# Performance work log

Hardware: AMD Instinct MI355X
Metric: run time of the kernel (lower is better)

## Reference

```python
import jax, jax.numpy as jnp
import numpy as np

EPS = 1e-12  # torch F.normalize eps

def _normalize(x):
    # L2-normalize along last dim, matching F.normalize(dim=-1)
    n = jnp.linalg.norm(x, axis=-1, keepdims=True)
    return x / jnp.maximum(n, EPS)

def setup_inputs() -> dict:
    key = jax.random.key(0)
    k1, k2, k3 = jax.random.split(key, 3)
    B, K, D = 32768, 8, 256
    return {
        "drone_slots": jax.random.normal(k1, (B, K, D), dtype=jnp.float32),
        "sat_slots": jax.random.normal(k2, (B, K, D), dtype=jnp.float32),
        "labels": jax.random.randint(k3, (B,), 0, 1000, dtype=jnp.int64),
        "temperature": 0.1,
    }

def reference(drone_slots, sat_slots, labels, temperature):
    # labels are unused by the original math (targets are arange(K))
    ds = _normalize(drone_slots)  # [B,K,D]
    ss = _normalize(sat_slots)    # [B,K,D]
    logits = jnp.einsum("bkd,bjd->bkj", ds, ss) / temperature  # [B,K,K]
    # cross_entropy with targets = arange(K): positive is the diagonal
    lse = jax.nn.logsumexp(logits, axis=-1)                      # [B,K]
    pos = jnp.diagonal(logits, axis1=-2, axis2=-1)               # [B,K]
    ce_per_sample = jnp.mean(lse - pos, axis=-1)                 # [B], per-sample mean-reduced CE
    return jnp.mean(ce_per_sample)                               # average over batch
```

## Files before the change

kernel.cpp:

```cpp
#include <hip/hip_runtime.h>
#include <hip/hip_bf16.h>


typedef __attribute__((ext_vector_type(8))) short bf16x8;
typedef __attribute__((ext_vector_type(4))) float f32x4;

union BFPack { bf16x8 v; __hip_bfloat162 h[4]; };

__device__ inline bf16x8 pack8(const float4& lo, const float4& hi) {
  BFPack u;
  u.h[0] = __float22bfloat162_rn(make_float2(lo.x, lo.y));
  u.h[1] = __float22bfloat162_rn(make_float2(lo.z, lo.w));
  u.h[2] = __float22bfloat162_rn(make_float2(hi.x, hi.y));
  u.h[3] = __float22bfloat162_rn(make_float2(hi.z, hi.w));
  return u.v;
}

extern "C" __global__ __launch_bounds__(256, 2)
void slot_ce_mfma(const float* __restrict__ ds, const float* __restrict__ ss,
                  const float* __restrict__ tptr, float* __restrict__ ws,
                  int ntiles) {
  const int lane = threadIdx.x & 63;
  const int wid  = blockIdx.x * 4 + (threadIdx.x >> 6);
  const int m = lane & 15;
  const int h = lane >> 4;
  const float inv_t = 1.0f / tptr[0];

  float loss = 0.0f;

  if (wid < ntiles) {
    const float4* pa = (const float4*)(ds + (size_t)wid * 4096);
    const float4* pb = (const float4*)(ss + (size_t)wid * 4096);
    const int base = m * 64 + h * 2;

    float4 A[16], S[16];
#pragma unroll
    for (int kb = 0; kb < 8; ++kb) {
      A[2 * kb]     = pa[base + kb * 8];
      A[2 * kb + 1] = pa[base + kb * 8 + 1];
      S[2 * kb]     = pb[base + kb * 8];
      S[2 * kb + 1] = pb[base + kb * 8 + 1];
    }

    f32x4 acc = {0.f, 0.f, 0.f, 0.f};
    float ssqA = 0.f, ssqS = 0.f;
#pragma unroll
    for (int kb = 0; kb < 8; ++kb) {
      float4 a0 = A[2 * kb], a1 = A[2 * kb + 1];
      float4 s0 = S[2 * kb], s1 = S[2 * kb + 1];

      ssqA += a0.x*a0.x + a0.y*a0.y + a0.z*a0.z + a0.w*a0.w
            + a1.x*a1.x + a1.y*a1.y + a1.z*a1.z + a1.w*a1.w;
      ssqS += s0.x*s0.x + s0.y*s0.y + s0.z*s0.z + s0.w*s0.w
            + s1.x*s1.x + s1.y*s1.y + s1.z*s1.z + s1.w*s1.w;

      acc = __builtin_amdgcn_mfma_f32_16x16x32_bf16(
          pack8(a0, a1), pack8(s0, s1), acc, 0, 0, 0);
    }

    ssqA += __shfl_xor(ssqA, 16, 64);
    ssqA += __shfl_xor(ssqA, 32, 64);
    ssqS += __shfl_xor(ssqS, 16, 64);
    ssqS += __shfl_xor(ssqS, 32, 64);
    float na0 = __shfl(ssqA, h * 4 + 0, 64);
    float na1 = __shfl(ssqA, h * 4 + 1, 64);
    float na2 = __shfl(ssqA, h * 4 + 2, 64);
    float na3 = __shfl(ssqA, h * 4 + 3, 64);

    float lg0 = acc[0] * rsqrtf(na0 * ssqS) * inv_t;
    float lg1 = acc[1] * rsqrtf(na1 * ssqS) * inv_t;
    float lg2 = acc[2] * rsqrtf(na2 * ssqS) * inv_t;
    float lg3 = acc[3] * rsqrtf(na3 * ssqS) * inv_t;

    float c = 0.0f;
#pragma unroll
    for (int r = 0; r < 4; ++r) {
      float lg = r == 0 ? lg0 : r == 1 ? lg1 : r == 2 ? lg2 : lg3;
      float mx = lg;
      mx = fmaxf(mx, __shfl_xor(mx, 1, 64));
      mx = fmaxf(mx, __shfl_xor(mx, 2, 64));
      mx = fmaxf(mx, __shfl_xor(mx, 4, 64));
      float e = __expf(lg - mx);
      e += __shfl_xor(e, 1, 64);
      e += __shfl_xor(e, 2, 64);
      e += __shfl_xor(e, 4, 64);
      float lse = mx + __logf(e);
      c += lse * 0.125f;
      if (4 * h + r == m) c -= lg;
    }
    if ((m >= 8) == (h >= 2)) loss = c;
  }

#pragma unroll
  for (int o = 32; o >= 1; o >>= 1) loss += __shfl_xor(loss, o, 64);
  __shared__ float red[4];
  if (lane == 0) red[threadIdx.x >> 6] = loss;
  __syncthreads();
  if (threadIdx.x == 0)
    ws[blockIdx.x] = (red[0] + red[1]) + (red[2] + red[3]);
}

extern "C" __global__ __launch_bounds__(256)
void slot_ce_finish(const float* __restrict__ ws, float* __restrict__ out,
                    int nparts, float scale) {
  __shared__ float red[256];
  float s = 0.0f;
  for (int i = threadIdx.x; i < nparts; i += 256) s += ws[i];
  red[threadIdx.x] = s;
  __syncthreads();
  for (int o = 128; o >= 1; o >>= 1) {
    if ((int)threadIdx.x < o) red[threadIdx.x] += red[threadIdx.x + o];
    __syncthreads();
  }
  if (threadIdx.x == 0) out[0] = red[0] * scale;
}

extern "C" void kernel_launch(void* const* d_in, const int* in_sizes, int n_in,
                              void* d_out, int out_size, void* d_ws, size_t ws_size,
                              hipStream_t stream) {
  const float* ds   = (const float*)d_in[0];
  const float* ss   = (const float*)d_in[1];
  const float* tptr = (const float*)d_in[3];
  float* out = (float*)d_out;
  float* ws  = (float*)d_ws;

  const int B      = in_sizes[0] / (8 * 256);
  const int ntiles = B / 2;
  const int blocks = (ntiles + 3) / 4;

  slot_ce_mfma<<<blocks, 256, 0, stream>>>(ds, ss, tptr, ws, ntiles);
  const float scale = 1.0f / (8.0f * (float)B);
  slot_ce_finish<<<1, 256, 0, stream>>>(ws, out, blocks, scale);
}
```

Baseline: 106.5 us.

## Stage slot tiles through LDS via direct global-to-LDS loads and fuse final reduction

Replaces the register-held 32 float4 loads per lane with global_load_lds transfers into a swizzled per-wave LDS region, processing the 256-wide dimension in four chunks and raising launch bounds to 5 blocks per CU. The final cross-block reduction is folded into the main kernel with an atomic ticket counter so the last block sums the partials, which drops the second launch but adds a memset. The per-chunk load then wait-for-all-loads pattern serializes memory and compute within a wave and relies on occupancy to hide latency. The LDS reads are missing a wait before the final chunk is consumed, and reuse of the buffer between chunks depends on manual waitcnt placement.

```diff
diff --git a/kernel.cpp b/kernel.cpp
--- a/kernel.cpp
+++ b/kernel.cpp
@@ -16,46 +16,69 @@
   return u.v;
 }
 
-extern "C" __global__ __launch_bounds__(256, 2)
-void slot_ce_mfma(const float* __restrict__ ds, const float* __restrict__ ss,
-                  const float* __restrict__ tptr, float* __restrict__ ws,
-                  int ntiles) {
-  const int lane = threadIdx.x & 63;
-  const int wid  = blockIdx.x * 4 + (threadIdx.x >> 6);
-  const int m = lane & 15;
-  const int h = lane >> 4;
+#define GLL16(gaddr, laddr)                                                    \
+  __builtin_amdgcn_global_load_lds(                                            \
+      (const __attribute__((address_space(1))) void*)(gaddr),                  \
+      (__attribute__((address_space(3))) void*)(laddr), 16, 0, 0)
+
+extern "C" __global__ __launch_bounds__(256, 5)
+void slot_ce_fused(const float* __restrict__ ds, const float* __restrict__ ss,
+                   const float* __restrict__ tptr, float* __restrict__ ws,
+                   unsigned* __restrict__ counter, float* __restrict__ out,
+                   int ntiles, int nblocks, float scale) {
+  __shared__ char lds[32768];
+  const int tid  = threadIdx.x;
+  const int lane = tid & 63;
+  const int wv   = tid >> 6;
+  const int wid  = blockIdx.x * 4 + wv;
+  const int m  = lane & 15;
+  const int h  = lane >> 4;
   const float inv_t = 1.0f / tptr[0];
 
+  char* wreg = &lds[wv * 8192];
   float loss = 0.0f;
 
   if (wid < ntiles) {
-    const float4* pa = (const float4*)(ds + (size_t)wid * 4096);
-    const float4* pb = (const float4*)(ss + (size_t)wid * 4096);
-    const int base = m * 64 + h * 2;
+    const char* gA = (const char*)ds + (size_t)wid * 16384;
+    const char* gB = (const char*)ss + (size_t)wid * 16384;
 
-    float4 A[16], S[16];
+    int srcoff[4];
 #pragma unroll
-    for (int kb = 0; kb < 8; ++kb) {
-      A[2 * kb]     = pa[base + kb * 8];
-      A[2 * kb + 1] = pa[base + kb * 8 + 1];
-      S[2 * kb]     = pb[base + kb * 8];
-      S[2 * kb + 1] = pb[base + kb * 8 + 1];
+    for (int j = 0; j < 4; ++j) {
+      const int row = j * 4 + (lane >> 4);
+      srcoff[j] = row * 1024 + ((m ^ (row & 7)) << 4);
     }
 
     f32x4 acc = {0.f, 0.f, 0.f, 0.f};
     float ssqA = 0.f, ssqS = 0.f;
+
 #pragma unroll
-    for (int kb = 0; kb < 8; ++kb) {
-      float4 a0 = A[2 * kb], a1 = A[2 * kb + 1];
-      float4 s0 = S[2 * kb], s1 = S[2 * kb + 1];
+    for (int ks = 0; ks < 4; ++ks) {
+      const int kofs = ks * 256;
+#pragma unroll
+      for (int j = 0; j < 4; ++j) GLL16(gA + srcoff[j] + kofs, wreg + j * 1024);
+#pragma unroll
+      for (int j = 0; j < 4; ++j) GLL16(gB + srcoff[j] + kofs, wreg + 4096 + j * 1024);
+      asm volatile("s_waitcnt vmcnt(0)" ::: "memory");
 
-      ssqA += a0.x*a0.x + a0.y*a0.y + a0.z*a0.z + a0.w*a0.w
-            + a1.x*a1.x + a1.y*a1.y + a1.z*a1.z + a1.w*a1.w;
-      ssqS += s0.x*s0.x + s0.y*s0.y + s0.z*s0.z + s0.w*s0.w
-            + s1.x*s1.x + s1.y*s1.y + s1.z*s1.z + s1.w*s1.w;
+#pragma unroll
+      for (int kb = 0; kb < 2; ++kb) {
+        const int sbase = kb * 8 + h * 2;
+        const int swz = m & 7;
+        const float4 a0 = *(const float4*)(wreg +        m * 256 + (((sbase + 0) ^ swz) << 4));
+        const float4 a1 = *(const float4*)(wreg +        m * 256 + (((sbase + 1) ^ swz) << 4));
+        const float4 s0 = *(const float4*)(wreg + 4096 + m * 256 + (((sbase + 0) ^ swz) << 4));
+        const float4 s1 = *(const float4*)(wreg + 4096 + m * 256 + (((sbase + 1) ^ swz) << 4));
 
-      acc = __builtin_amdgcn_mfma_f32_16x16x32_bf16(
-          pack8(a0, a1), pack8(s0, s1), acc, 0, 0, 0);
+        ssqA += a0.x*a0.x + a0.y*a0.y + a0.z*a0.z + a0.w*a0.w
+              + a1.x*a1.x + a1.y*a1.y + a1.z*a1.z + a1.w*a1.w;
+        ssqS += s0.x*s0.x + s0.y*s0.y + s0.z*s0.z + s0.w*s0.w
+              + s1.x*s1.x + s1.y*s1.y + s1.z*s1.z + s1.w*s1.w;
+
+        acc = __builtin_amdgcn_mfma_f32_16x16x32_bf16(
+            pack8(a0, a1), pack8(s0, s1), acc, 0, 0, 0);
+      }
+      if (ks < 3) asm volatile("s_waitcnt lgkmcnt(0)" ::: "memory");
     }
 
     ssqA += __shfl_xor(ssqA, 16, 64);
@@ -93,26 +116,33 @@
 
 #pragma unroll
   for (int o = 32; o >= 1; o >>= 1) loss += __shfl_xor(loss, o, 64);
-  __shared__ float red[4];
-  if (lane == 0) red[threadIdx.x >> 6] = loss;
+  float* redp = (float*)lds;
   __syncthreads();
-  if (threadIdx.x == 0)
-    ws[blockIdx.x] = (red[0] + red[1]) + (red[2] + red[3]);
-}
+  if (lane == 0) redp[wv] = loss;
+  __syncthreads();
+  if (tid == 0) {
+    const float part = (redp[0] + redp[1]) + (redp[2] + redp[3]);
+    atomicExch(&ws[blockIdx.x], part);
+    __threadfence();
+    unsigned old = atomicAdd(counter, 1u);
+    *(unsigned*)(lds + 16) = (old == (unsigned)(nblocks - 1)) ? 1u : 0u;
+  }
+  __syncthreads();
+  const bool last = *(volatile unsigned*)(lds + 16) != 0u;
+  __syncthreads();
 
-extern "C" __global__ __launch_bounds__(256)
-void slot_ce_finish(const float* __restrict__ ws, float* __restrict__ out,
-                    int nparts, float scale) {
-  __shared__ float red[256];
-  float s = 0.0f;
-  for (int i = threadIdx.x; i < nparts; i += 256) s += ws[i];
-  red[threadIdx.x] = s;
-  __syncthreads();
-  for (int o = 128; o >= 1; o >>= 1) {
-    if ((int)threadIdx.x < o) red[threadIdx.x] += red[threadIdx.x + o];
+  if (last) {
+    __threadfence();
+    float s = 0.0f;
+    for (int i = tid; i < nblocks; i += 256) s += ws[i];
+    ((float*)lds)[tid] = s;
     __syncthreads();
+    for (int o = 128; o >= 1; o >>= 1) {
+      if (tid < o) ((float*)lds)[tid] += ((float*)lds)[tid + o];
+      __syncthreads();
+    }
+    if (tid == 0) out[0] = ((float*)lds)[0] * scale;
   }
-  if (threadIdx.x == 0) out[0] = red[0] * scale;
 }
 
 extern "C" void kernel_launch(void* const* d_in, const int* in_sizes, int n_in,
@@ -123,12 +153,14 @@
   const float* tptr = (const float*)d_in[3];
   float* out = (float*)d_out;
   float* ws  = (float*)d_ws;
+  unsigned* counter = (unsigned*)((char*)d_ws + 16384);
 
-  const int B      = in_sizes[0] / (8 * 256);
-  const int ntiles = B / 2;
-  const int blocks = (ntiles + 3) / 4;
+  const int B       = in_sizes[0] / (8 * 256);
+  const int ntiles  = B / 2;
+  const int nblocks = (ntiles + 3) / 4;
 
-  slot_ce_mfma<<<blocks, 256, 0, stream>>>(ds, ss, tptr, ws, ntiles);
+  hipMemsetAsync(counter, 0, sizeof(unsigned), stream);
   const float scale = 1.0f / (8.0f * (float)B);
-  slot_ce_finish<<<1, 256, 0, stream>>>(ws, out, blocks, scale);
+  slot_ce_fused<<<nblocks, 256, 0, stream>>>(ds, ss, tptr, ws, counter, out,
+                                             ntiles, nblocks, scale);
 }
```

Measured after the change: 301.3 us. +183.0%, slower.
